# Optimization experiments

Hardware: AMD Instinct MI355X
Metric: run time of the kernel (lower is better)

## Reference

```python
import jax, jax.numpy as jnp
import numpy as np

L, B, F, E, H, V, NL, K = 32, 128, 4096, 512, 512, 50000, 2, 20


def setup_inputs() -> dict:
    key = jax.random.key(0)
    ks = jax.random.split(key, 9)
    return {
        "dialog_encoder_inputs": jax.random.randint(ks[0], (L, B), 0, V),
        "fact_inputs": jax.random.normal(ks[1], (B, F, E), dtype=jnp.float32),
        "h": jax.random.normal(ks[2], (NL, B, H), dtype=jnp.float32),
        "c": jax.random.normal(ks[3], (NL, B, H), dtype=jnp.float32),
        "enc_emb": jax.random.normal(ks[4], (V, E), dtype=jnp.float32) * 0.02,
        "Aw": jax.random.normal(ks[5], (H, E), dtype=jnp.float32) * 0.04,
        "Ab": jnp.zeros((H,), dtype=jnp.float32),
        "Cw": jax.random.normal(ks[6], (H, E), dtype=jnp.float32) * 0.04,
        "Cb": jnp.zeros((H,), dtype=jnp.float32),
        "top_k": K,
    }


def reference(dialog_encoder_inputs, fact_inputs, h, c, enc_emb, Aw, Ab, Cw, Cb, top_k):
    # --- get_top_k_fact_average: embed dialog, score facts, gather top-k ---
    q = enc_emb[dialog_encoder_inputs].mean(axis=0)                # [B, E] mean-pooled query
    scores = jnp.einsum('be,bfe->bf', q, fact_inputs)              # [B, F] similarity
    _, idx = jax.lax.top_k(scores, top_k)                          # [B, K]
    topf = jnp.take_along_axis(fact_inputs, idx[:, :, None], axis=1)  # [B, K, E]

    # --- facts_forward: memory-network style hidden-state update ---
    fact_M = jnp.einsum('bke,he->bkh', topf, Aw) + Ab              # fact_linearA
    fact_C = jnp.einsum('bke,he->bkh', topf, Cw) + Cb              # fact_linearC

    def update(u):  # u: [NL, B, H]
        P = jax.nn.softmax(jnp.einsum('bke,lbe->lbk', topf, u), axis=-1)  # attn over facts
        o = jnp.einsum('lbk,bke->lbe', P, topf)                           # weighted fact avg
        return o + u

    return update(h), update(c), fact_M, fact_C
```

## Files before the change

### kernel.cpp

```cpp
#include <hip/hip_runtime.h>
#include <float.h>
#include <math.h>

#define LL 32
#define BB 128
#define FF 4096
#define EE 512
#define HH 512
#define NLAYER 2
#define KK 20

typedef float f4 __attribute__((ext_vector_type(4)));
typedef short bf16x8 __attribute__((ext_vector_type(8)));
typedef float f32x4 __attribute__((ext_vector_type(4)));

__device__ inline unsigned short bf16rne(float x) {
    unsigned u = __float_as_uint(x);
    u += 0x7fff + ((u >> 16) & 1);
    return (unsigned short)(u >> 16);
}

__device__ inline unsigned long long packkey(float v, int fidx) {
    unsigned u = __float_as_uint(v);
    u ^= ((int)u >> 31) | 0x80000000u;
    return ((unsigned long long)u << 32) | (unsigned)(FF - 1 - fidx);
}

__global__ __launch_bounds__(256) void prep_kernel(const int* __restrict__ tok,
                                                   const float* __restrict__ emb,
                                                   float* __restrict__ q,
                                                   const float* __restrict__ Aw,
                                                   const float* __restrict__ Cw,
                                                   unsigned short* __restrict__ Wbf) {
    int bid = blockIdx.x;
    if (bid < 256) {
        int b = bid >> 1, eh = bid & 1;
        __shared__ int ts[LL];
        if (threadIdx.x < LL) ts[threadIdx.x] = tok[threadIdx.x * BB + b];
        __syncthreads();
        int e = eh * 256 + threadIdx.x;
        float acc = 0.f;
        #pragma unroll
        for (int l = 0; l < LL; ++l) acc += emb[(long)ts[l] * EE + e];
        q[b * EE + e] = acc * (1.0f / LL);
    } else {
        int cid = bid - 256;
        int matY = cid >> 8;
        int blkX = cid & 255;
        const float* W = matY ? Cw : Aw;
        unsigned short* dst = Wbf + (size_t)matY * HH * EE;
        int i = (blkX * 256 + threadIdx.x) * 4;
        float4 v = *(const float4*)(W + i);
        ushort4 o;
        o.x = bf16rne(v.x); o.y = bf16rne(v.y); o.z = bf16rne(v.z); o.w = bf16rne(v.w);
        *(ushort4*)(dst + i) = o;
    }
}

__global__ __launch_bounds__(256) void scores_kernel(const float* __restrict__ q,
                                                     const float* __restrict__ fact,
                                                     float* __restrict__ scores) {
    int b = blockIdx.y;
    int wave = threadIdx.x >> 6;
    int lane = threadIdx.x & 63;
    const f4* qv = (const f4*)(q + b * EE);
    f4 qa = qv[lane];
    f4 qb = qv[64 + lane];
    int f0 = (blockIdx.x * 4 + wave) * 8;
    float d[8];
    #pragma unroll
    for (int i = 0; i < 8; ++i) {
        const f4* fv = (const f4*)(fact + ((long)b * FF + f0 + i) * EE);
        f4 fa = __builtin_nontemporal_load(fv + lane);
        f4 fb = __builtin_nontemporal_load(fv + 64 + lane);
        f4 p = qa * fa + qb * fb;
        d[i] = p.x + p.y + p.z + p.w;
    }
    bool h32 = lane & 32;
    float e0, e1, e2, e3;
    {
        float s0 = __shfl_xor(d[0], 32), s1 = __shfl_xor(d[1], 32);
        float s2 = __shfl_xor(d[2], 32), s3 = __shfl_xor(d[3], 32);
        float s4 = __shfl_xor(d[4], 32), s5 = __shfl_xor(d[5], 32);
        float s6 = __shfl_xor(d[6], 32), s7 = __shfl_xor(d[7], 32);
        e0 = h32 ? d[4] + s4 : d[0] + s0;
        e1 = h32 ? d[5] + s5 : d[1] + s1;
        e2 = h32 ? d[6] + s6 : d[2] + s2;
        e3 = h32 ? d[7] + s7 : d[3] + s3;
    }
    bool h16 = lane & 16;
    float g0, g1;
    {
        float s0 = __shfl_xor(e0, 16), s1 = __shfl_xor(e1, 16);
        float s2 = __shfl_xor(e2, 16), s3 = __shfl_xor(e3, 16);
        g0 = h16 ? e2 + s2 : e0 + s0;
        g1 = h16 ? e3 + s3 : e1 + s1;
    }
    bool h8 = lane & 8;
    float hs;
    {
        float s0 = __shfl_xor(g0, 8), s1 = __shfl_xor(g1, 8);
        hs = h8 ? g1 + s1 : g0 + s0;
    }
    hs += __shfl_xor(hs, 4);
    hs += __shfl_xor(hs, 2);
    hs += __shfl_xor(hs, 1);
    if ((lane & 7) == 0) scores[b * FF + f0 + ((lane >> 3) & 7)] = hs;
}

__global__ __launch_bounds__(256) void topk_update_kernel(const float* __restrict__ scores,
                                                          const float* __restrict__ fact,
                                                          const float* __restrict__ hin,
                                                          const float* __restrict__ cin,
                                                          unsigned short* __restrict__ topfb,
                                                          float* __restrict__ out) {
    int b = blockIdx.x;
    __shared__ float tf[KK][EE];
    __shared__ unsigned long long wkeys[4 * KK];
    __shared__ int sel[KK];
    int t = threadIdx.x;
    int wave = t >> 6, lane = t & 63;

    {
        const float4* sv = (const float4*)(scores + b * FF);
        unsigned long long keys[16];
        #pragma unroll
        for (int s = 0; s < 4; ++s) {
            int j = wave * 256 + s * 64 + lane;
            float4 v = sv[j];
            float vc[4] = {v.x, v.y, v.z, v.w};
            #pragma unroll
            for (int c = 0; c < 4; ++c)
                keys[s * 4 + c] = packkey(vc[c], 4 * j + c);
        }
        unsigned long long mykey = 0;
        for (int it = 0; it < KK; ++it) {
            unsigned long long best = keys[0];
            #pragma unroll
            for (int i = 1; i < 16; ++i) best = keys[i] > best ? keys[i] : best;
            #pragma unroll
            for (int off = 32; off > 0; off >>= 1) {
                unsigned long long o = __shfl_xor(best, off, 64);
                if (o > best) best = o;
            }
            if (lane == it) mykey = best;
            #pragma unroll
            for (int i = 0; i < 16; ++i)
                if (keys[i] == best) keys[i] = 0;
        }
        if (lane < KK) wkeys[wave * KK + lane] = mykey;
    }
    __syncthreads();

    if (wave == 0) {
        unsigned long long k0 = wkeys[lane];
        unsigned long long k1 = lane < 4 * KK - 64 ? wkeys[64 + lane] : 0;
        for (int it = 0; it < KK; ++it) {
            unsigned long long best = k0 > k1 ? k0 : k1;
            #pragma unroll
            for (int off = 32; off > 0; off >>= 1) {
                unsigned long long o = __shfl_xor(best, off, 64);
                if (o > best) best = o;
            }
            if (lane == 0) sel[it] = FF - 1 - (int)(best & 0xFFFFFFFFu);
            if (k0 == best) k0 = 0;
            if (k1 == best) k1 = 0;
        }
    }
    __syncthreads();

    for (int kk = 0; kk < KK; kk += 2) {
        int k = kk + (t >> 7);
        int e = t & 127;
        int src = sel[k];
        float4 v = *(const float4*)(fact + (((long)b * FF + src) * EE) + e * 4);
        *(float4*)&tf[k][e * 4] = v;
        ushort4 o;
        o.x = bf16rne(v.x); o.y = bf16rne(v.y); o.z = bf16rne(v.z); o.w = bf16rne(v.w);
        *(ushort4*)(topfb + ((size_t)b * KK + k) * EE + e * 4) = o;
    }
    __syncthreads();

    const float* u = (wave < 2 ? hin : cin) + ((size_t)(wave & 1) * BB + b) * EE;
    const float4* uv = (const float4*)u;
    float4 ua = uv[lane], ub = uv[64 + lane];
    float sk[KK];
    #pragma unroll
    for (int k = 0; k < KK; ++k) {
        const float4* tv = (const float4*)&tf[k][0];
        float4 ta = tv[lane], tb = tv[64 + lane];
        float d = ua.x * ta.x + ua.y * ta.y + ua.z * ta.z + ua.w * ta.w
                + ub.x * tb.x + ub.y * tb.y + ub.z * tb.z + ub.w * tb.w;
        #pragma unroll
        for (int off = 32; off > 0; off >>= 1) d += __shfl_xor(d, off, 64);
        sk[k] = d;
    }
    float m = sk[0];
    #pragma unroll
    for (int k = 1; k < KK; ++k) m = fmaxf(m, sk[k]);
    float sum = 0.f;
    #pragma unroll
    for (int k = 0; k < KK; ++k) { sk[k] = __expf(sk[k] - m); sum += sk[k]; }
    float inv = 1.f / sum;
    float4 oa = {0, 0, 0, 0}, ob = {0, 0, 0, 0};
    #pragma unroll
    for (int k = 0; k < KK; ++k) {
        float p = sk[k] * inv;
        const float4* tv = (const float4*)&tf[k][0];
        float4 ta = tv[lane], tb = tv[64 + lane];
        oa.x += p * ta.x; oa.y += p * ta.y; oa.z += p * ta.z; oa.w += p * ta.w;
        ob.x += p * tb.x; ob.y += p * tb.y; ob.z += p * tb.z; ob.w += p * tb.w;
    }
    oa.x += ua.x; oa.y += ua.y; oa.z += ua.z; oa.w += ua.w;
    ob.x += ub.x; ob.y += ub.y; ob.z += ub.z; ob.w += ub.w;
    float* obase = out + (size_t)(wave < 2 ? 0 : NLAYER * BB * HH)
                       + ((size_t)(wave & 1) * BB + b) * HH;
    float4* ov = (float4*)obase;
    ov[lane] = oa;
    ov[64 + lane] = ob;
}

__global__ __launch_bounds__(256) void factmc_kernel(const unsigned short* __restrict__ topfb,
                                                     const unsigned short* __restrict__ Wbf,
                                                     const float* __restrict__ Ab,
                                                     const float* __restrict__ Cb,
                                                     float* __restrict__ out) {
    int b = blockIdx.x, mat = blockIdx.y;
    const unsigned short* W = Wbf + (size_t)mat * HH * EE;
    const float* bias = mat ? Cb : Ab;
    float* O = out + (size_t)2 * NLAYER * BB * HH
                   + (size_t)mat * BB * KK * HH + (size_t)b * KK * HH;

    __shared__ unsigned short tf[32 * EE];
    {
        const unsigned short* src = topfb + (size_t)b * KK * EE;
        for (int ib = threadIdx.x; ib < KK * EE / 8; ib += 256) {
            int row = ib >> 6;
            int cb = ib & 63;
            float4 v = *(const float4*)(src + row * EE + cb * 8);
            int byte = (row * 1024 + cb * 16) ^ ((row & 7) << 4);
            *(float4*)((char*)tf + byte) = v;
        }
    }
    __syncthreads();

    int wave = threadIdx.x >> 6, lane = threadIdx.x & 63;
    int lrow = lane & 15, lk = lane >> 4;
    f32x4 acc[2][8];
    #pragma unroll
    for (int m = 0; m < 2; ++m)
        #pragma unroll
        for (int n = 0; n < 8; ++n) acc[m][n] = (f32x4){0, 0, 0, 0};

    const unsigned short* wbase = W + (size_t)(wave * 128 + lrow) * EE + lk * 8;

    #pragma unroll 2
    for (int ks = 0; ks < 16; ++ks) {
        int col2 = (ks * 32 + lk * 8) * 2;
        int byte0 = (lrow * 1024 + col2) ^ ((lrow & 7) << 4);
        bf16x8 a0 = *(const bf16x8*)((const char*)tf + byte0);
        int r1 = 16 + lrow;
        int byte1 = (r1 * 1024 + col2) ^ ((r1 & 7) << 4);
        bf16x8 a1 = *(const bf16x8*)((const char*)tf + byte1);
        #pragma unroll
        for (int n = 0; n < 8; ++n) {
            bf16x8 bfrag = *(const bf16x8*)(wbase + (size_t)n * 16 * EE + ks * 32);
            acc[0][n] = __builtin_amdgcn_mfma_f32_16x16x32_bf16(a0, bfrag, acc[0][n], 0, 0, 0);
            acc[1][n] = __builtin_amdgcn_mfma_f32_16x16x32_bf16(a1, bfrag, acc[1][n], 0, 0, 0);
        }
    }

    #pragma unroll
    for (int n = 0; n < 8; ++n) {
        int h = wave * 128 + n * 16 + lrow;
        float bv = bias[h];
        #pragma unroll
        for (int r = 0; r < 4; ++r) {
            int k0 = lk * 4 + r;
            O[(size_t)k0 * HH + h] = acc[0][n][r] + bv;
            int k1 = 16 + lk * 4 + r;
            if (k1 < KK) O[(size_t)k1 * HH + h] = acc[1][n][r] + bv;
        }
    }
}

extern "C" void kernel_launch(void* const* d_in, const int* in_sizes, int n_in,
                              void* d_out, int out_size, void* d_ws, size_t ws_size,
                              hipStream_t stream) {
    const int* tok = (const int*)d_in[0];
    const float* fact = (const float*)d_in[1];
    const float* hin = (const float*)d_in[2];
    const float* cin = (const float*)d_in[3];
    const float* emb = (const float*)d_in[4];
    const float* Aw = (const float*)d_in[5];
    const float* Ab = (const float*)d_in[6];
    const float* Cw = (const float*)d_in[7];
    const float* Cb = (const float*)d_in[8];
    float* out = (float*)d_out;

    float* ws = (float*)d_ws;
    float* q = ws;
    float* scores = ws + 65536;
    unsigned short* topfb = (unsigned short*)(ws + 65536 + 524288);
    unsigned short* Wbf = (unsigned short*)(ws + 65536 + 524288 + 655360);

    prep_kernel<<<768, 256, 0, stream>>>(tok, emb, q, Aw, Cw, Wbf);
    scores_kernel<<<dim3(FF / 32, BB), 256, 0, stream>>>(q, fact, scores);
    topk_update_kernel<<<BB, 256, 0, stream>>>(scores, fact, hin, cin, topfb, out);
    factmc_kernel<<<dim3(BB, 2), 256, 0, stream>>>(topfb, Wbf, Ab, Cb, out);
}
```

Measured before the change: 227.6 us.

## Fuse top-k/update with fact linear GEMM and move weight conversion into scores kernel

```diff
diff --git a/kernel.cpp b/kernel.cpp
--- a/kernel.cpp
+++ b/kernel.cpp
@@ -26,27 +26,30 @@
     return ((unsigned long long)u << 32) | (unsigned)(FF - 1 - fidx);
 }
 
-__global__ __launch_bounds__(256) void prep_kernel(const int* __restrict__ tok,
-                                                   const float* __restrict__ emb,
-                                                   float* __restrict__ q,
-                                                   const float* __restrict__ Aw,
-                                                   const float* __restrict__ Cw,
-                                                   unsigned short* __restrict__ Wbf) {
+__global__ __launch_bounds__(256) void q_kernel(const int* __restrict__ tok,
+                                                const float* __restrict__ emb,
+                                                float* __restrict__ q) {
+    int b = blockIdx.x >> 1, eh = blockIdx.x & 1;
+    __shared__ int ts[LL];
+    if (threadIdx.x < LL) ts[threadIdx.x] = tok[threadIdx.x * BB + b];
+    __syncthreads();
+    int e = eh * 256 + threadIdx.x;
+    float acc = 0.f;
+    #pragma unroll
+    for (int l = 0; l < LL; ++l) acc += emb[(long)ts[l] * EE + e];
+    q[b * EE + e] = acc * (1.0f / LL);
+}
+
+__global__ __launch_bounds__(256) void scores_conv_kernel(const float* __restrict__ q,
+                                                          const float* __restrict__ fact,
+                                                          float* __restrict__ scores,
+                                                          const float* __restrict__ Aw,
+                                                          const float* __restrict__ Cw,
+                                                          unsigned short* __restrict__ Wbf) {
     int bid = blockIdx.x;
-    if (bid < 256) {
-        int b = bid >> 1, eh = bid & 1;
-        __shared__ int ts[LL];
-        if (threadIdx.x < LL) ts[threadIdx.x] = tok[threadIdx.x * BB + b];
-        __syncthreads();
-        int e = eh * 256 + threadIdx.x;
-        float acc = 0.f;
-        #pragma unroll
-        for (int l = 0; l < LL; ++l) acc += emb[(long)ts[l] * EE + e];
-        q[b * EE + e] = acc * (1.0f / LL);
-    } else {
-        int cid = bid - 256;
-        int matY = cid >> 8;
-        int blkX = cid & 255;
+    if (bid < 512) {
+        int matY = bid >> 8;
+        int blkX = bid & 255;
         const float* W = matY ? Cw : Aw;
         unsigned short* dst = Wbf + (size_t)matY * HH * EE;
         int i = (blkX * 256 + threadIdx.x) * 4;
@@ -54,19 +57,16 @@
         ushort4 o;
         o.x = bf16rne(v.x); o.y = bf16rne(v.y); o.z = bf16rne(v.z); o.w = bf16rne(v.w);
         *(ushort4*)(dst + i) = o;
-    }
-}
-
-__global__ __launch_bounds__(256) void scores_kernel(const float* __restrict__ q,
-                                                     const float* __restrict__ fact,
-                                                     float* __restrict__ scores) {
-    int b = blockIdx.y;
+        return;
+    }
+    int sid = bid - 512;
+    int b = sid >> 7, chunkf = sid & 127;
     int wave = threadIdx.x >> 6;
     int lane = threadIdx.x & 63;
     const f4* qv = (const f4*)(q + b * EE);
     f4 qa = qv[lane];
     f4 qb = qv[64 + lane];
-    int f0 = (blockIdx.x * 4 + wave) * 8;
+    int f0 = (chunkf * 4 + wave) * 8;
     float d[8];
     #pragma unroll
     for (int i = 0; i < 8; ++i) {
@@ -108,14 +108,17 @@
     if ((lane & 7) == 0) scores[b * FF + f0 + ((lane >> 3) & 7)] = hs;
 }
 
-__global__ __launch_bounds__(256) void topk_update_kernel(const float* __restrict__ scores,
-                                                          const float* __restrict__ fact,
-                                                          const float* __restrict__ hin,
-                                                          const float* __restrict__ cin,
-                                                          unsigned short* __restrict__ topfb,
-                                                          float* __restrict__ out) {
-    int b = blockIdx.x;
+__global__ __launch_bounds__(256) void fused_tail_kernel(const float* __restrict__ scores,
+                                                         const float* __restrict__ fact,
+                                                         const float* __restrict__ hin,
+                                                         const float* __restrict__ cin,
+                                                         const unsigned short* __restrict__ Wbf,
+                                                         const float* __restrict__ Ab,
+                                                         const float* __restrict__ Cb,
+                                                         float* __restrict__ out) {
+    int b = blockIdx.x, mat = blockIdx.y;
     __shared__ float tf[KK][EE];
+    __shared__ unsigned short tfb[32 * EE];
     __shared__ unsigned long long wkeys[4 * KK];
     __shared__ int sel[KK];
     int t = threadIdx.x;
@@ -177,109 +180,92 @@
         *(float4*)&tf[k][e * 4] = v;
         ushort4 o;
         o.x = bf16rne(v.x); o.y = bf16rne(v.y); o.z = bf16rne(v.z); o.w = bf16rne(v.w);
-        *(ushort4*)(topfb + ((size_t)b * KK + k) * EE + e * 4) = o;
-    }
-    __syncthreads();
-
-    const float* u = (wave < 2 ? hin : cin) + ((size_t)(wave & 1) * BB + b) * EE;
-    const float4* uv = (const float4*)u;
-    float4 ua = uv[lane], ub = uv[64 + lane];
-    float sk[KK];
-    #pragma unroll
-    for (int k = 0; k < KK; ++k) {
-        const float4* tv = (const float4*)&tf[k][0];
-        float4 ta = tv[lane], tb = tv[64 + lane];
-        float d = ua.x * ta.x + ua.y * ta.y + ua.z * ta.z + ua.w * ta.w
-                + ub.x * tb.x + ub.y * tb.y + ub.z * tb.z + ub.w * tb.w;
-        #pragma unroll
-        for (int off = 32; off > 0; off >>= 1) d += __shfl_xor(d, off, 64);
-        sk[k] = d;
-    }
-    float m = sk[0];
-    #pragma unroll
-    for (int k = 1; k < KK; ++k) m = fmaxf(m, sk[k]);
-    float sum = 0.f;
-    #pragma unroll
-    for (int k = 0; k < KK; ++k) { sk[k] = __expf(sk[k] - m); sum += sk[k]; }
-    float inv = 1.f / sum;
-    float4 oa = {0, 0, 0, 0}, ob = {0, 0, 0, 0};
-    #pragma unroll
-    for (int k = 0; k < KK; ++k) {
-        float p = sk[k] * inv;
-        const float4* tv = (const float4*)&tf[k][0];
-        float4 ta = tv[lane], tb = tv[64 + lane];
-        oa.x += p * ta.x; oa.y += p * ta.y; oa.z += p * ta.z; oa.w += p * ta.w;
-        ob.x += p * tb.x; ob.y += p * tb.y; ob.z += p * tb.z; ob.w += p * tb.w;
-    }
-    oa.x += ua.x; oa.y += ua.y; oa.z += ua.z; oa.w += ua.w;
-    ob.x += ub.x; ob.y += ub.y; ob.z += ub.z; ob.w += ub.w;
-    float* obase = out + (size_t)(wave < 2 ? 0 : NLAYER * BB * HH)
-                       + ((size_t)(wave & 1) * BB + b) * HH;
-    float4* ov = (float4*)obase;
-    ov[lane] = oa;
-    ov[64 + lane] = ob;
-}
-
-__global__ __launch_bounds__(256) void factmc_kernel(const unsigned short* __restrict__ topfb,
-                                                     const unsigned short* __restrict__ Wbf,
-                                                     const float* __restrict__ Ab,
-                                                     const float* __restrict__ Cb,
-                                                     float* __restrict__ out) {
-    int b = blockIdx.x, mat = blockIdx.y;
-    const unsigned short* W = Wbf + (size_t)mat * HH * EE;
-    const float* bias = mat ? Cb : Ab;
-    float* O = out + (size_t)2 * NLAYER * BB * HH
-                   + (size_t)mat * BB * KK * HH + (size_t)b * KK * HH;
-
-    __shared__ unsigned short tf[32 * EE];
-    {
-        const unsigned short* src = topfb + (size_t)b * KK * EE;
-        for (int ib = threadIdx.x; ib < KK * EE / 8; ib += 256) {
-            int row = ib >> 6;
-            int cb = ib & 63;
-            float4 v = *(const float4*)(src + row * EE + cb * 8);
-            int byte = (row * 1024 + cb * 16) ^ ((row & 7) << 4);
-            *(float4*)((char*)tf + byte) = v;
-        }
-    }
-    __syncthreads();
-
-    int wave = threadIdx.x >> 6, lane = threadIdx.x & 63;
-    int lrow = lane & 15, lk = lane >> 4;
-    f32x4 acc[2][8];
-    #pragma unroll
-    for (int m = 0; m < 2; ++m)
-        #pragma unroll
-        for (int n = 0; n < 8; ++n) acc[m][n] = (f32x4){0, 0, 0, 0};
-
-    const unsigned short* wbase = W + (size_t)(wave * 128 + lrow) * EE + lk * 8;
-
-    #pragma unroll 2
-    for (int ks = 0; ks < 16; ++ks) {
-        int col2 = (ks * 32 + lk * 8) * 2;
-        int byte0 = (lrow * 1024 + col2) ^ ((lrow & 7) << 4);
-        bf16x8 a0 = *(const bf16x8*)((const char*)tf + byte0);
-        int r1 = 16 + lrow;
-        int byte1 = (r1 * 1024 + col2) ^ ((r1 & 7) << 4);
-        bf16x8 a1 = *(const bf16x8*)((const char*)tf + byte1);
+        int byte = (k * 1024 + e * 8) ^ ((k & 7) << 4);
+        *(ushort4*)((char*)tfb + byte) = o;
+    }
+    __syncthreads();
+
+    if ((mat == 0) ? (wave < 2) : (wave >= 2)) {
+        const float* u = (wave < 2 ? hin : cin) + ((size_t)(wave & 1) * BB + b) * EE;
+        const float4* uv = (const float4*)u;
+        float4 ua = uv[lane], ub = uv[64 + lane];
+        float sk[KK];
+        #pragma unroll
+        for (int k = 0; k < KK; ++k) {
+            const float4* tv = (const float4*)&tf[k][0];
+            float4 ta = tv[lane], tb = tv[64 + lane];
+            float d = ua.x * ta.x + ua.y * ta.y + ua.z * ta.z + ua.w * ta.w
+                    + ub.x * tb.x + ub.y * tb.y + ub.z * tb.z + ub.w * tb.w;
+            #pragma unroll
+            for (int off = 32; off > 0; off >>= 1) d += __shfl_xor(d, off, 64);
+            sk[k] = d;
+        }
+        float m = sk[0];
+        #pragma unroll
+        for (int k = 1; k < KK; ++k) m = fmaxf(m, sk[k]);
+        float sum = 0.f;
+        #pragma unroll
+        for (int k = 0; k < KK; ++k) { sk[k] = __expf(sk[k] - m); sum += sk[k]; }
+        float inv = 1.f / sum;
+        float4 oa = {0, 0, 0, 0}, ob = {0, 0, 0, 0};
+        #pragma unroll
+        for (int k = 0; k < KK; ++k) {
+            float p = sk[k] * inv;
+            const float4* tv = (const float4*)&tf[k][0];
+            float4 ta = tv[lane], tb = tv[64 + lane];
+            oa.x += p * ta.x; oa.y += p * ta.y; oa.z += p * ta.z; oa.w += p * ta.w;
+            ob.x += p * tb.x; ob.y += p * tb.y; ob.z += p * tb.z; ob.w += p * tb.w;
+        }
+        oa.x += ua.x; oa.y += ua.y; oa.z += ua.z; oa.w += ua.w;
+        ob.x += ub.x; ob.y += ub.y; ob.z += ub.z; ob.w += ub.w;
+        float* obase = out + (size_t)(wave < 2 ? 0 : NLAYER * BB * HH)
+                           + ((size_t)(wave & 1) * BB + b) * HH;
+        float4* ov = (float4*)obase;
+        ov[lane] = oa;
+        ov[64 + lane] = ob;
+    }
+
+    {
+        const unsigned short* W = Wbf + (size_t)mat * HH * EE;
+        const float* bias = mat ? Cb : Ab;
+        float* O = out + (size_t)2 * NLAYER * BB * HH
+                       + (size_t)mat * BB * KK * HH + (size_t)b * KK * HH;
+        int lrow = lane & 15, lk = lane >> 4;
+        f32x4 acc[2][8];
+        #pragma unroll
+        for (int m = 0; m < 2; ++m)
+            #pragma unroll
+            for (int n = 0; n < 8; ++n) acc[m][n] = (f32x4){0, 0, 0, 0};
+
+        const unsigned short* wbase = W + (size_t)(wave * 128 + lrow) * EE + lk * 8;
+
+        #pragma unroll 2
+        for (int ks = 0; ks < 16; ++ks) {
+            int col2 = (ks * 32 + lk * 8) * 2;
+            int byte0 = (lrow * 1024 + col2) ^ ((lrow & 7) << 4);
+            bf16x8 a0 = *(const bf16x8*)((const char*)tfb + byte0);
+            int r1 = 16 + lrow;
+            int byte1 = (r1 * 1024 + col2) ^ ((r1 & 7) << 4);
+            bf16x8 a1 = *(const bf16x8*)((const char*)tfb + byte1);
+            #pragma unroll
+            for (int n = 0; n < 8; ++n) {
+                bf16x8 bfrag = *(const bf16x8*)(wbase + (size_t)n * 16 * EE + ks * 32);
+                acc[0][n] = __builtin_amdgcn_mfma_f32_16x16x32_bf16(a0, bfrag, acc[0][n], 0, 0, 0);
+                acc[1][n] = __builtin_amdgcn_mfma_f32_16x16x32_bf16(a1, bfrag, acc[1][n], 0, 0, 0);
+            }
+        }
+
         #pragma unroll
         for (int n = 0; n < 8; ++n) {
-            bf16x8 bfrag = *(const bf16x8*)(wbase + (size_t)n * 16 * EE + ks * 32);
-            acc[0][n] = __builtin_amdgcn_mfma_f32_16x16x32_bf16(a0, bfrag, acc[0][n], 0, 0, 0);
-            acc[1][n] = __builtin_amdgcn_mfma_f32_16x16x32_bf16(a1, bfrag, acc[1][n], 0, 0, 0);
-        }
-    }
-
-    #pragma unroll
-    for (int n = 0; n < 8; ++n) {
-        int h = wave * 128 + n * 16 + lrow;
-        float bv = bias[h];
-        #pragma unroll
-        for (int r = 0; r < 4; ++r) {
-            int k0 = lk * 4 + r;
-            O[(size_t)k0 * HH + h] = acc[0][n][r] + bv;
-            int k1 = 16 + lk * 4 + r;
-            if (k1 < KK) O[(size_t)k1 * HH + h] = acc[1][n][r] + bv;
+            int h = wave * 128 + n * 16 + lrow;
+            float bv = bias[h];
+            #pragma unroll
+            for (int r = 0; r < 4; ++r) {
+                int k0 = lk * 4 + r;
+                O[(size_t)k0 * HH + h] = acc[0][n][r] + bv;
+                int k1 = 16 + lk * 4 + r;
+                if (k1 < KK) O[(size_t)k1 * HH + h] = acc[1][n][r] + bv;
+            }
         }
     }
 }
@@ -301,11 +287,9 @@
     float* ws = (float*)d_ws;
     float* q = ws;
     float* scores = ws + 65536;
-    unsigned short* topfb = (unsigned short*)(ws + 65536 + 524288);
-    unsigned short* Wbf = (unsigned short*)(ws + 65536 + 524288 + 655360);
-
-    prep_kernel<<<768, 256, 0, stream>>>(tok, emb, q, Aw, Cw, Wbf);
-    scores_kernel<<<dim3(FF / 32, BB), 256, 0, stream>>>(q, fact, scores);
-    topk_update_kernel<<<BB, 256, 0, stream>>>(scores, fact, hin, cin, topfb, out);
-    factmc_kernel<<<dim3(BB, 2), 256, 0, stream>>>(topfb, Wbf, Ab, Cb, out);
-}
+    unsigned short* Wbf = (unsigned short*)(ws + 65536 + 524288);
+
+    q_kernel<<<256, 256, 0, stream>>>(tok, emb, q);
+    scores_conv_kernel<<<512 + BB * 128, 256, 0, stream>>>(q, fact, scores, Aw, Cw, Wbf);
+    fused_tail_kernel<<<dim3(BB, 2), 256, 0, stream>>>(scores, fact, hin, cin, Wbf, Ab, Cb, out);
+}
```

Measured after the change: 221.3 us. -2.8%, faster.
